# Optimization experiments

Measured on AMD Instinct MI355X. Metric: run time of the kernel, lower is better.

Reference implementation:

```python
import jax, jax.numpy as jnp
import numpy as np

PLANE_SIZE = 512
N_LEVELS = 8
FEATURE_DIM = 16
N_PTS = 524288


def setup_inputs() -> dict:
    key = jax.random.key(0)
    k1, k2, k3 = jax.random.split(key, 3)
    x = jax.random.uniform(k1, (N_PTS, 3), dtype=jnp.float32)
    # per-point float mip level bias in [0, n_levels-1]
    level = jax.random.uniform(k2, (N_PTS, 1), dtype=jnp.float32) * (N_LEVELS - 1)
    fm = jax.random.uniform(k3, (3, PLANE_SIZE, PLANE_SIZE, FEATURE_DIM),
                            minval=-0.01, maxval=0.01, dtype=jnp.float32)
    return {"x": x, "level": level, "fm": fm, "n_levels": N_LEVELS}


def _bilinear(flat_pyr, offsets, sizes, uv, lvl_i):
    # flat_pyr: (3, T, C) concatenated mip levels; uv: (3, N, 2); lvl_i: (3, N) int32
    size = sizes[lvl_i]                      # (3, N) texture size at this mip
    fsize = size.astype(uv.dtype)
    px = uv[..., 0] * fsize - 0.5            # u -> width axis (nvdiffrast convention)
    py = uv[..., 1] * fsize - 0.5            # v -> height axis
    x0 = jnp.floor(px)
    y0 = jnp.floor(py)
    fx = (px - x0)[..., None]
    fy = (py - y0)[..., None]
    x0i = x0.astype(jnp.int32)
    y0i = y0.astype(jnp.int32)
    xa = jnp.clip(x0i, 0, size - 1)          # boundary_mode='clamp'
    xb = jnp.clip(x0i + 1, 0, size - 1)
    ya = jnp.clip(y0i, 0, size - 1)
    yb = jnp.clip(y0i + 1, 0, size - 1)
    base = offsets[lvl_i]
    p = jnp.arange(3)[:, None]
    g = lambda yy, xx: flat_pyr[p, base + yy * size + xx]   # (3, N, C) gather
    f00 = g(ya, xa); f01 = g(ya, xb); f10 = g(yb, xa); f11 = g(yb, xb)
    return (f00 * (1 - fx) + f01 * fx) * (1 - fy) + (f10 * (1 - fx) + f11 * fx) * fy


def reference(x, level, fm, n_levels):
    N = x.shape[0]
    C = fm.shape[-1]
    # build mip pyramid via 2x2 box filter (nvdiffrast auto-mips)
    levels = [fm]
    for _ in range(n_levels - 1):
        t = levels[-1]
        s = t.shape[1]
        levels.append(t.reshape(3, s // 2, 2, s // 2, 2, C).mean(axis=(2, 4)))
    sizes_list = [l.shape[1] for l in levels]
    offsets = jnp.asarray(np.cumsum([0] + [s * s for s in sizes_list[:-1]]), jnp.int32)
    sizes = jnp.asarray(sizes_list, jnp.int32)
    flat_pyr = jnp.concatenate([l.reshape(3, -1, C) for l in levels], axis=1)  # (3, T, C)
    # tri-plane decomposition: plane0 sees (y,z), plane1 (x,z), plane2 (x,y)
    uv = jnp.stack([x[:, [1, 2]], x[:, [0, 2]], x[:, [0, 1]]], axis=0)  # (3, N, 2)
    max_mip = n_levels - 1
    lvl = jnp.clip(jnp.broadcast_to(level.reshape(1, N), (3, N)), 0.0, float(max_mip))
    l0 = jnp.floor(lvl)
    f = (lvl - l0)[..., None]                # (3, N, 1) level fraction
    l0i = l0.astype(jnp.int32)
    l1i = jnp.minimum(l0i + 1, max_mip)
    s0 = _bilinear(flat_pyr, offsets, sizes, uv, l0i)
    s1 = _bilinear(flat_pyr, offsets, sizes, uv, l1i)
    enc = s0 * (1 - f) + s1 * f              # (3, N, C) trilinear (mip-lerped)
    # permute(1,2,0,3).view(N, 3C): per point, concat plane0|plane1|plane2 features
    return jnp.transpose(enc, (1, 0, 2)).reshape(N, 3 * C)
```

## Files before the change

kernel.cpp:

```cpp
#include <hip/hip_runtime.h>
#include <hip/hip_fp16.h>


typedef float  f4v   __attribute__((ext_vector_type(4)));
typedef unsigned int u32x2 __attribute__((ext_vector_type(2)));

#define FM_PLANE_STRIDE (262144 * 16)
#define WS_PLANE_STRIDE (87376 * 16)
#define PSTRIDE_H (349520 * 16)
#define WS_H_BYTES (3ull * PSTRIDE_H * 2ull)

__device__ __forceinline__ unsigned lvl_off(int l) {
    return (1048576u - (1048576u >> (2 * l))) / 3u;
}

__device__ __forceinline__ f4v ld4(const float* p) {
    return *reinterpret_cast<const f4v*>(p);
}
__device__ __forceinline__ f4v ld4nt(const float* p) {
    return __builtin_nontemporal_load(reinterpret_cast<const f4v*>(p));
}
__device__ __forceinline__ void st4(float* p, f4v v) {
    *reinterpret_cast<f4v*>(p) = v;
}
__device__ __forceinline__ void st4nt(float* p, f4v v) {
    __builtin_nontemporal_store(v, reinterpret_cast<f4v*>(p));
}
__device__ __forceinline__ f4v ldraw_h(const __half* p) {
    return *reinterpret_cast<const f4v*>(p);
}
__device__ __forceinline__ u32x2 pack4(f4v v) {
    __half2 lo = __floats2half2_rn(v.x, v.y);
    __half2 hi = __floats2half2_rn(v.z, v.w);
    u32x2 r;
    r.x = *reinterpret_cast<unsigned*>(&lo);
    r.y = *reinterpret_cast<unsigned*>(&hi);
    return r;
}
__device__ __forceinline__ f4v h4f(const __half* p) {
    u32x2 u = *reinterpret_cast<const u32x2*>(p);
    unsigned a0 = u.x, a1 = u.y;
    __half2 lo = *reinterpret_cast<__half2*>(&a0);
    __half2 hi = *reinterpret_cast<__half2*>(&a1);
    float2 flo = __half22float2(lo), fhi = __half22float2(hi);
    f4v r; r.x = flo.x; r.y = flo.y; r.z = fhi.x; r.w = fhi.y;
    return r;
}
__device__ __forceinline__ float2 up2(float rawcomp) {
    unsigned u = __float_as_uint(rawcomp);
    __half2 hh = *reinterpret_cast<__half2*>(&u);
    return __half22float2(hh);
}


__global__ __launch_bounds__(256) void mip_convert_l1(
    const float* __restrict__ fm, __half* __restrict__ wsh)
{
    int t = blockIdx.x * 256 + threadIdx.x;
    const int p = blockIdx.y;
    const int q = t & 3, idx = t >> 2;
    const int y = idx >> 8, x = idx & 255;
    const float* sp = fm + (size_t)p * FM_PLANE_STRIDE
                         + ((size_t)(2 * y) * 512 + 2 * x) * 16 + q * 4;
    f4v a = ld4nt(sp);
    f4v b = ld4nt(sp + 16);
    f4v c = ld4nt(sp + 512 * 16);
    f4v d = ld4nt(sp + 512 * 16 + 16);
    __half* L0 = wsh + (size_t)p * PSTRIDE_H;
    size_t o00 = ((size_t)(2 * y) * 512 + 2 * x) * 16 + q * 4;
    *reinterpret_cast<u32x2*>(L0 + o00)                = pack4(a);
    *reinterpret_cast<u32x2*>(L0 + o00 + 16)           = pack4(b);
    *reinterpret_cast<u32x2*>(L0 + o00 + 512 * 16)     = pack4(c);
    *reinterpret_cast<u32x2*>(L0 + o00 + 512 * 16 + 16) = pack4(d);
    f4v m = (a + b + c + d) * 0.25f;
    __half* L1 = wsh + (size_t)p * PSTRIDE_H + (size_t)262144 * 16;
    *reinterpret_cast<u32x2*>(L1 + ((size_t)y * 256 + x) * 16 + q * 4) = pack4(m);
}

__global__ __launch_bounds__(256) void mip_tail_h(__half* __restrict__ wsh)
{
    const int tile = blockIdx.x;
    const int q    = blockIdx.y;
    const int p    = blockIdx.z;
    const int ty = tile >> 2, tx = tile & 3;
    const int tid = threadIdx.x;

    __shared__ f4v A[32 * 32];
    __shared__ f4v B[16 * 16];

    __half* plane = wsh + (size_t)p * PSTRIDE_H;
    const __half* L1 = plane + (size_t)lvl_off(1) * 16;
    __half* L2 = plane + (size_t)lvl_off(2) * 16;
    __half* L3 = plane + (size_t)lvl_off(3) * 16;
    __half* L4 = plane + (size_t)lvl_off(4) * 16;
    __half* L5 = plane + (size_t)lvl_off(5) * 16;
    __half* L6 = plane + (size_t)lvl_off(6) * 16;
    __half* L7 = plane + (size_t)lvl_off(7) * 16;

    #pragma unroll
    for (int k = 0; k < 4; ++k) {
        int li = tid + k * 256;
        int ly = li >> 5, lx = li & 31;
        int gy = ty * 32 + ly, gx = tx * 32 + lx;
        const __half* sp = L1 + ((size_t)(2 * gy) * 256 + 2 * gx) * 16 + q * 4;
        f4v r = (h4f(sp) + h4f(sp + 16) + h4f(sp + 256 * 16) + h4f(sp + 256 * 16 + 16)) * 0.25f;
        A[li] = r;
        *reinterpret_cast<u32x2*>(L2 + ((size_t)gy * 128 + gx) * 16 + q * 4) = pack4(r);
    }
    __syncthreads();

    {
        int ly = tid >> 4, lx = tid & 15;
        f4v r = (A[(2 * ly) * 32 + 2 * lx]     + A[(2 * ly) * 32 + 2 * lx + 1] +
                 A[(2 * ly + 1) * 32 + 2 * lx] + A[(2 * ly + 1) * 32 + 2 * lx + 1]) * 0.25f;
        B[tid] = r;
        *reinterpret_cast<u32x2*>(L3 + ((size_t)(ty * 16 + ly) * 64 + tx * 16 + lx) * 16 + q * 4) = pack4(r);
    }
    __syncthreads();

    if (tid < 64) {
        int ly = tid >> 3, lx = tid & 7;
        f4v r = (B[(2 * ly) * 16 + 2 * lx]     + B[(2 * ly) * 16 + 2 * lx + 1] +
                 B[(2 * ly + 1) * 16 + 2 * lx] + B[(2 * ly + 1) * 16 + 2 * lx + 1]) * 0.25f;
        A[tid] = r;
        *reinterpret_cast<u32x2*>(L4 + ((size_t)(ty * 8 + ly) * 32 + tx * 8 + lx) * 16 + q * 4) = pack4(r);
    }
    __syncthreads();

    if (tid < 16) {
        int ly = tid >> 2, lx = tid & 3;
        f4v r = (A[(2 * ly) * 8 + 2 * lx]     + A[(2 * ly) * 8 + 2 * lx + 1] +
                 A[(2 * ly + 1) * 8 + 2 * lx] + A[(2 * ly + 1) * 8 + 2 * lx + 1]) * 0.25f;
        B[tid] = r;
        *reinterpret_cast<u32x2*>(L5 + ((size_t)(ty * 4 + ly) * 16 + tx * 4 + lx) * 16 + q * 4) = pack4(r);
    }
    __syncthreads();

    if (tid < 4) {
        int ly = tid >> 1, lx = tid & 1;
        f4v r = (B[(2 * ly) * 4 + 2 * lx]     + B[(2 * ly) * 4 + 2 * lx + 1] +
                 B[(2 * ly + 1) * 4 + 2 * lx] + B[(2 * ly + 1) * 4 + 2 * lx + 1]) * 0.25f;
        A[tid] = r;
        *reinterpret_cast<u32x2*>(L6 + ((size_t)(ty * 2 + ly) * 8 + tx * 2 + lx) * 16 + q * 4) = pack4(r);
    }
    __syncthreads();

    if (tid == 0) {
        f4v r = (A[0] + A[1] + A[2] + A[3]) * 0.25f;
        *reinterpret_cast<u32x2*>(L7 + ((size_t)ty * 4 + tx) * 16 + q * 4) = pack4(r);
    }
}

__device__ __forceinline__ void bilerp8(
    const __half* __restrict__ wsh, int p, int l, float u, float v, int h, float* o)
{
    const int sz = 512 >> l;
    const float fsz = (float)sz;
    float px = u * fsz - 0.5f;
    float py = v * fsz - 0.5f;
    float xf = floorf(px), yf = floorf(py);
    float fx = px - xf, fy = py - yf;
    int xi = (int)xf, yi = (int)yf;
    int xa = min(max(xi, 0), sz - 1);
    int xb = min(xi + 1, sz - 1);
    int ya = min(max(yi, 0), sz - 1);
    int yb = min(yi + 1, sz - 1);
    const __half* base = wsh + (size_t)p * PSTRIDE_H + (size_t)lvl_off(l) * 16 + h * 8;
    const __half* r0 = base + (size_t)(ya * sz) * 16;
    const __half* r1 = base + (size_t)(yb * sz) * 16;
    f4v q00 = ldraw_h(r0 + (size_t)xa * 16);
    f4v q01 = ldraw_h(r0 + (size_t)xb * 16);
    f4v q10 = ldraw_h(r1 + (size_t)xa * 16);
    f4v q11 = ldraw_h(r1 + (size_t)xb * 16);
    float gx = 1.f - fx, gy = 1.f - fy;
    float w00 = gx * gy, w01 = fx * gy, w10 = gx * fy, w11 = fx * fy;
    #pragma unroll
    for (int i = 0; i < 4; ++i) {
        float2 a = up2(q00[i]), b = up2(q01[i]), c = up2(q10[i]), d = up2(q11[i]);
        o[2 * i]     = a.x * w00 + b.x * w01 + c.x * w10 + d.x * w11;
        o[2 * i + 1] = a.y * w00 + b.y * w01 + c.y * w10 + d.y * w11;
    }
}

__global__ __launch_bounds__(256) void trimip_sample_h(
    const float* __restrict__ xyz, const float* __restrict__ level,
    const __half* __restrict__ wsh, float* __restrict__ out, int N)
{
    int t = blockIdx.x * blockDim.x + threadIdx.x;
    if (t >= N * 6) return;
    const int h = t & 1;
    const int r = t >> 1;
    const int n = r / 3;
    const int p = r - n * 3;

    const float c0 = xyz[n * 3 + 0];
    const float c1 = xyz[n * 3 + 1];
    const float c2 = xyz[n * 3 + 2];
    const float u = (p == 0) ? c1 : c0;
    const float v = (p == 2) ? c1 : c2;

    float lv = level[n];
    lv = fminf(fmaxf(lv, 0.f), 7.f);
    float lf = floorf(lv);
    float f = lv - lf;
    int l0 = (int)lf;
    int l1 = min(l0 + 1, 7);

    float s0[8], s1[8];
    bilerp8(wsh, p, l0, u, v, h, s0);
    bilerp8(wsh, p, l1, u, v, h, s1);
    float g = 1.f - f;
    f4v oa, ob;
    #pragma unroll
    for (int i = 0; i < 4; ++i) {
        oa[i] = s0[i] * g + s1[i] * f;
        ob[i] = s0[4 + i] * g + s1[4 + i] * f;
    }
    st4nt(out + (size_t)t * 8, oa);
    st4nt(out + (size_t)t * 8 + 4, ob);
}


__device__ __forceinline__ f4v avg4(f4v a, f4v b, f4v c, f4v d) {
    return (a + b + c + d) * 0.25f;
}

__global__ __launch_bounds__(256) void mip_build_f(
    const float* __restrict__ src, float* __restrict__ dst)
{
    int t = blockIdx.x * blockDim.x + threadIdx.x;
    const int p = blockIdx.y;
    const int q = t & 3, idx = t >> 2;
    const int y = idx >> 8, x = idx & 255;
    const float* sp = src + (size_t)p * FM_PLANE_STRIDE
                          + ((size_t)(2 * y) * 512 + 2 * x) * 16 + q * 4;
    f4v r = avg4(ld4(sp), ld4(sp + 16), ld4(sp + 512 * 16), ld4(sp + 512 * 16 + 16));
    st4(dst + (size_t)p * WS_PLANE_STRIDE + ((size_t)y * 256 + x) * 16 + q * 4, r);
}

__global__ __launch_bounds__(256) void mip_tail_f(float* __restrict__ mips)
{
    const int tile = blockIdx.x, q = blockIdx.y, p = blockIdx.z;
    const int ty = tile >> 2, tx = tile & 3;
    const int tid = threadIdx.x;
    __shared__ f4v A[32 * 32];
    __shared__ f4v B[16 * 16];
    float* plane = mips + (size_t)p * WS_PLANE_STRIDE;
    const float* L1 = plane;
    float* L2 = plane + (size_t)65536 * 16;
    float* L3 = plane + (size_t)81920 * 16;
    float* L4 = plane + (size_t)86016 * 16;
    float* L5 = plane + (size_t)87040 * 16;
    float* L6 = plane + (size_t)87296 * 16;
    float* L7 = plane + (size_t)87360 * 16;

    #pragma unroll
    for (int k = 0; k < 4; ++k) {
        int li = tid + k * 256;
        int ly = li >> 5, lx = li & 31;
        int gy = ty * 32 + ly, gx = tx * 32 + lx;
        const float* sp = L1 + ((size_t)(2 * gy) * 256 + 2 * gx) * 16 + q * 4;
        f4v r = avg4(ld4(sp), ld4(sp + 16), ld4(sp + 256 * 16), ld4(sp + 256 * 16 + 16));
        A[li] = r;
        st4(L2 + ((size_t)gy * 128 + gx) * 16 + q * 4, r);
    }
    __syncthreads();
    {
        int ly = tid >> 4, lx = tid & 15;
        f4v r = avg4(A[(2 * ly) * 32 + 2 * lx],     A[(2 * ly) * 32 + 2 * lx + 1],
                     A[(2 * ly + 1) * 32 + 2 * lx], A[(2 * ly + 1) * 32 + 2 * lx + 1]);
        B[tid] = r;
        st4(L3 + ((size_t)(ty * 16 + ly) * 64 + tx * 16 + lx) * 16 + q * 4, r);
    }
    __syncthreads();
    if (tid < 64) {
        int ly = tid >> 3, lx = tid & 7;
        f4v r = avg4(B[(2 * ly) * 16 + 2 * lx],     B[(2 * ly) * 16 + 2 * lx + 1],
                     B[(2 * ly + 1) * 16 + 2 * lx], B[(2 * ly + 1) * 16 + 2 * lx + 1]);
        A[tid] = r;
        st4(L4 + ((size_t)(ty * 8 + ly) * 32 + tx * 8 + lx) * 16 + q * 4, r);
    }
    __syncthreads();
    if (tid < 16) {
        int ly = tid >> 2, lx = tid & 3;
        f4v r = avg4(A[(2 * ly) * 8 + 2 * lx],     A[(2 * ly) * 8 + 2 * lx + 1],
                     A[(2 * ly + 1) * 8 + 2 * lx], A[(2 * ly + 1) * 8 + 2 * lx + 1]);
        B[tid] = r;
        st4(L5 + ((size_t)(ty * 4 + ly) * 16 + tx * 4 + lx) * 16 + q * 4, r);
    }
    __syncthreads();
    if (tid < 4) {
        int ly = tid >> 1, lx = tid & 1;
        f4v r = avg4(B[(2 * ly) * 4 + 2 * lx],     B[(2 * ly) * 4 + 2 * lx + 1],
                     B[(2 * ly + 1) * 4 + 2 * lx], B[(2 * ly + 1) * 4 + 2 * lx + 1]);
        A[tid] = r;
        st4(L6 + ((size_t)(ty * 2 + ly) * 8 + tx * 2 + lx) * 16 + q * 4, r);
    }
    __syncthreads();
    if (tid == 0) {
        f4v r = avg4(A[0], A[1], A[2], A[3]);
        st4(L7 + ((size_t)ty * 4 + tx) * 16 + q * 4, r);
    }
}

__device__ __forceinline__ f4v bilerp_f(
    const float* __restrict__ fm, const float* __restrict__ mips,
    int p, int l, float u, float v, int q)
{
    const int sz = 512 >> l;
    const float fsz = (float)sz;
    float px = u * fsz - 0.5f;
    float py = v * fsz - 0.5f;
    float xf = floorf(px), yf = floorf(py);
    float fx = px - xf, fy = py - yf;
    int xi = (int)xf, yi = (int)yf;
    int xa = min(max(xi, 0), sz - 1);
    int xb = min(xi + 1, sz - 1);
    int ya = min(max(yi, 0), sz - 1);
    int yb = min(yi + 1, sz - 1);
    const float* base;
    if (l == 0) {
        base = fm + (size_t)p * FM_PLANE_STRIDE;
    } else {
        unsigned off = (262144u - ((unsigned)(sz * sz) << 2)) / 3u;
        base = mips + (size_t)p * WS_PLANE_STRIDE + (size_t)off * 16;
    }
    const float* r0 = base + (size_t)(ya * sz) * 16 + q * 4;
    const float* r1 = base + (size_t)(yb * sz) * 16 + q * 4;
    f4v f00 = ld4(r0 + xa * 16);
    f4v f01 = ld4(r0 + xb * 16);
    f4v f10 = ld4(r1 + xa * 16);
    f4v f11 = ld4(r1 + xb * 16);
    float gx = 1.f - fx, gy = 1.f - fy;
    return (f00 * gx + f01 * fx) * gy + (f10 * gx + f11 * fx) * fy;
}

__global__ __launch_bounds__(256) void trimip_sample_f(
    const float* __restrict__ xyz, const float* __restrict__ level,
    const float* __restrict__ fm, const float* __restrict__ mips,
    float* __restrict__ out, int N)
{
    int t = blockIdx.x * blockDim.x + threadIdx.x;
    if (t >= N * 12) return;
    const int q = t & 3;
    const int r = t >> 2;
    const int n = r / 3;
    const int p = r - n * 3;
    const float c0 = xyz[n * 3 + 0];
    const float c1 = xyz[n * 3 + 1];
    const float c2 = xyz[n * 3 + 2];
    const float u = (p == 0) ? c1 : c0;
    const float v = (p == 2) ? c1 : c2;
    float lv = level[n];
    lv = fminf(fmaxf(lv, 0.f), 7.f);
    float lf = floorf(lv);
    float f = lv - lf;
    int l0 = (int)lf;
    int l1 = min(l0 + 1, 7);
    f4v s0 = bilerp_f(fm, mips, p, l0, u, v, q);
    f4v s1 = bilerp_f(fm, mips, p, l1, u, v, q);
    f4v o = s0 * (1.f - f) + s1 * f;
    st4nt(out + (size_t)t * 4, o);
}

extern "C" void kernel_launch(void* const* d_in, const int* in_sizes, int n_in,
                              void* d_out, int out_size, void* d_ws, size_t ws_size,
                              hipStream_t stream) {
    const float* xyz   = (const float*)d_in[0];
    const float* level = (const float*)d_in[1];
    const float* fm    = (const float*)d_in[2];
    float* out = (float*)d_out;
    const int N = in_sizes[1];

    if (ws_size >= WS_H_BYTES) {
        __half* wsh = (__half*)d_ws;
        mip_convert_l1<<<dim3(1024, 3), dim3(256), 0, stream>>>(fm, wsh);
        mip_tail_h<<<dim3(16, 4, 3), dim3(256), 0, stream>>>(wsh);
        const int total = N * 6;
        trimip_sample_h<<<(total + 255) / 256, 256, 0, stream>>>(xyz, level, wsh, out, N);
    } else {
        float* mips = (float*)d_ws;
        mip_build_f<<<dim3(1024, 3), dim3(256), 0, stream>>>(fm, mips);
        mip_tail_f<<<dim3(16, 4, 3), dim3(256), 0, stream>>>(mips);
        const int total = N * 12;
        trimip_sample_f<<<(total + 255) / 256, 256, 0, stream>>>(xyz, level, fm, mips, out, N);
    }
}
```

Measured before the change: 203.6 us.

## Stage coarsest mip levels in shared memory for the sampling kernel

Each block of the sampling kernel now copies mip levels 5–7 of all three planes (about 32 KB of fp16) into shared memory, and bilinear taps at those levels read from LDS instead of global memory. Block size grows from 256 to 512 threads to spread the staging cost over more points. The aim is to cut global and L2 traffic for the small, heavily reused coarse levels. The cost is a fixed 32 KB load plus a barrier per block, lower occupancy from the shared-memory footprint, and a divergent branch inside each bilinear lookup.

Result: no change. 201.2 us (-1.1%).

```diff
diff --git a/kernel.cpp b/kernel.cpp
--- a/kernel.cpp
+++ b/kernel.cpp
@@ -2,13 +2,15 @@
 #include <hip/hip_fp16.h>
 
 
-typedef float  f4v   __attribute__((ext_vector_type(4)));
+typedef float        f4v   __attribute__((ext_vector_type(4)));
 typedef unsigned int u32x2 __attribute__((ext_vector_type(2)));
+typedef unsigned int u32x4 __attribute__((ext_vector_type(4)));
 
 #define FM_PLANE_STRIDE (262144 * 16)
 #define WS_PLANE_STRIDE (87376 * 16)
 #define PSTRIDE_H (349520 * 16)
 #define WS_H_BYTES (3ull * PSTRIDE_H * 2ull)
+#define LVL5_OFF 349184u
 
 __device__ __forceinline__ unsigned lvl_off(int l) {
     return (1048576u - (1048576u >> (2 * l))) / 3u;
@@ -68,9 +70,9 @@
     f4v d = ld4nt(sp + 512 * 16 + 16);
     __half* L0 = wsh + (size_t)p * PSTRIDE_H;
     size_t o00 = ((size_t)(2 * y) * 512 + 2 * x) * 16 + q * 4;
-    *reinterpret_cast<u32x2*>(L0 + o00)                = pack4(a);
-    *reinterpret_cast<u32x2*>(L0 + o00 + 16)           = pack4(b);
-    *reinterpret_cast<u32x2*>(L0 + o00 + 512 * 16)     = pack4(c);
+    *reinterpret_cast<u32x2*>(L0 + o00)                 = pack4(a);
+    *reinterpret_cast<u32x2*>(L0 + o00 + 16)            = pack4(b);
+    *reinterpret_cast<u32x2*>(L0 + o00 + 512 * 16)      = pack4(c);
     *reinterpret_cast<u32x2*>(L0 + o00 + 512 * 16 + 16) = pack4(d);
     f4v m = (a + b + c + d) * 0.25f;
     __half* L1 = wsh + (size_t)p * PSTRIDE_H + (size_t)262144 * 16;
@@ -152,7 +154,8 @@
 }
 
 __device__ __forceinline__ void bilerp8(
-    const __half* __restrict__ wsh, int p, int l, float u, float v, int h, float* o)
+    const __half* __restrict__ wsh, const __half* __restrict__ lds_h,
+    int p, int l, float u, float v, int h, float* o)
 {
     const int sz = 512 >> l;
     const float fsz = (float)sz;
@@ -165,13 +168,25 @@
     int xb = min(xi + 1, sz - 1);
     int ya = min(max(yi, 0), sz - 1);
     int yb = min(yi + 1, sz - 1);
-    const __half* base = wsh + (size_t)p * PSTRIDE_H + (size_t)lvl_off(l) * 16 + h * 8;
-    const __half* r0 = base + (size_t)(ya * sz) * 16;
-    const __half* r1 = base + (size_t)(yb * sz) * 16;
-    f4v q00 = ldraw_h(r0 + (size_t)xa * 16);
-    f4v q01 = ldraw_h(r0 + (size_t)xb * 16);
-    f4v q10 = ldraw_h(r1 + (size_t)xa * 16);
-    f4v q11 = ldraw_h(r1 + (size_t)xb * 16);
+    f4v q00, q01, q10, q11;
+    if (l >= 5) {
+        const int sel = (l == 6) ? 256 : ((l == 7) ? 320 : 0);
+        const __half* base = lds_h + (size_t)(p * 336 + sel) * 16 + h * 8;
+        const __half* r0 = base + (ya * sz) * 16;
+        const __half* r1 = base + (yb * sz) * 16;
+        q00 = ldraw_h(r0 + xa * 16);
+        q01 = ldraw_h(r0 + xb * 16);
+        q10 = ldraw_h(r1 + xa * 16);
+        q11 = ldraw_h(r1 + xb * 16);
+    } else {
+        const __half* base = wsh + (size_t)p * PSTRIDE_H + (size_t)lvl_off(l) * 16 + h * 8;
+        const __half* r0 = base + (size_t)(ya * sz) * 16;
+        const __half* r1 = base + (size_t)(yb * sz) * 16;
+        q00 = ldraw_h(r0 + (size_t)xa * 16);
+        q01 = ldraw_h(r0 + (size_t)xb * 16);
+        q10 = ldraw_h(r1 + (size_t)xa * 16);
+        q11 = ldraw_h(r1 + (size_t)xb * 16);
+    }
     float gx = 1.f - fx, gy = 1.f - fy;
     float w00 = gx * gy, w01 = fx * gy, w10 = gx * fy, w11 = fx * fy;
     #pragma unroll
@@ -182,11 +197,21 @@
     }
 }
 
-__global__ __launch_bounds__(256) void trimip_sample_h(
+__global__ __launch_bounds__(512) void trimip_sample_h(
     const float* __restrict__ xyz, const float* __restrict__ level,
     const __half* __restrict__ wsh, float* __restrict__ out, int N)
 {
-    int t = blockIdx.x * blockDim.x + threadIdx.x;
+    __shared__ u32x4 lds[2016];
+    for (int uidx = threadIdx.x; uidx < 2016; uidx += 512) {
+        int p = uidx / 672;
+        int rem = uidx - p * 672;
+        lds[uidx] = *reinterpret_cast<const u32x4*>(
+            wsh + (size_t)p * PSTRIDE_H + (size_t)LVL5_OFF * 16 + (size_t)rem * 8);
+    }
+    __syncthreads();
+    const __half* lds_h = reinterpret_cast<const __half*>(lds);
+
+    int t = blockIdx.x * 512 + threadIdx.x;
     if (t >= N * 6) return;
     const int h = t & 1;
     const int r = t >> 1;
@@ -207,8 +232,8 @@
     int l1 = min(l0 + 1, 7);
 
     float s0[8], s1[8];
-    bilerp8(wsh, p, l0, u, v, h, s0);
-    bilerp8(wsh, p, l1, u, v, h, s1);
+    bilerp8(wsh, lds_h, p, l0, u, v, h, s0);
+    bilerp8(wsh, lds_h, p, l1, u, v, h, s1);
     float g = 1.f - f;
     f4v oa, ob;
     #pragma unroll
@@ -377,7 +402,7 @@
         mip_convert_l1<<<dim3(1024, 3), dim3(256), 0, stream>>>(fm, wsh);
         mip_tail_h<<<dim3(16, 4, 3), dim3(256), 0, stream>>>(wsh);
         const int total = N * 6;
-        trimip_sample_h<<<(total + 255) / 256, 256, 0, stream>>>(xyz, level, wsh, out, N);
+        trimip_sample_h<<<(total + 511) / 512, 512, 0, stream>>>(xyz, level, wsh, out, N);
     } else {
         float* mips = (float*)d_ws;
         mip_build_f<<<dim3(1024, 3), dim3(256), 0, stream>>>(fm, mips);
```

## Sort points by Morton key and level before sampling; read level 0 from fp32 input

Applied to the files above, without the earlier changes.

Adds a counting sort that bins points by a 16^3 Morton cell and integer mip level (histogram, single-block scan, atomic scatter), then samples in sorted order with a per-plane grid so neighbouring threads hit nearby texels. The fp16 copy of level 0 is no longer written; level 0 is bilinearly sampled directly from the fp32 input, which shrinks the pyramid build traffic. The sort is meant to improve cache locality of the random gathers. In exchange it adds four extra launches, atomics, and scattered output writes through the sort index.

After: 288.7 us. +41.8%, slower.

```diff
diff --git a/kernel.cpp b/kernel.cpp
--- a/kernel.cpp
+++ b/kernel.cpp
@@ -2,16 +2,18 @@
 #include <hip/hip_fp16.h>
 
 
-typedef float  f4v   __attribute__((ext_vector_type(4)));
+typedef float        f4v   __attribute__((ext_vector_type(4)));
 typedef unsigned int u32x2 __attribute__((ext_vector_type(2)));
 
 #define FM_PLANE_STRIDE (262144 * 16)
+#define PW_STRIDE_H (87376 * 16)
+#define PYR_BYTES 8388608ull
 #define WS_PLANE_STRIDE (87376 * 16)
-#define PSTRIDE_H (349520 * 16)
-#define WS_H_BYTES (3ull * PSTRIDE_H * 2ull)
-
-__device__ __forceinline__ unsigned lvl_off(int l) {
-    return (1048576u - (1048576u >> (2 * l))) / 3u;
+#define NBINS 32768
+
+__device__ __forceinline__ unsigned lvl_off_ws(int l) {
+    const int sz = 512 >> l;
+    return (262144u - ((unsigned)(sz * sz) << 2)) / 3u;
 }
 
 __device__ __forceinline__ f4v ld4(const float* p) {
@@ -51,10 +53,26 @@
     __half2 hh = *reinterpret_cast<__half2*>(&u);
     return __half22float2(hh);
 }
-
-
-__global__ __launch_bounds__(256) void mip_convert_l1(
-    const float* __restrict__ fm, __half* __restrict__ wsh)
+__device__ __forceinline__ unsigned part1by2(unsigned v) {
+    v = (v | (v << 16)) & 0x030000FFu;
+    v = (v | (v << 8))  & 0x0300F00Fu;
+    v = (v | (v << 4))  & 0x030C30C3u;
+    v = (v | (v << 2))  & 0x09249249u;
+    return v;
+}
+__device__ __forceinline__ unsigned point_key(float x, float y, float z, float lv) {
+    int xi = min(max((int)(x * 16.f), 0), 15);
+    int yi = min(max((int)(y * 16.f), 0), 15);
+    int zi = min(max((int)(z * 16.f), 0), 15);
+    int l0 = (int)lv;
+    unsigned m = part1by2((unsigned)xi) | (part1by2((unsigned)yi) << 1)
+               | (part1by2((unsigned)zi) << 2);
+    return ((unsigned)l0 << 12) | m;
+}
+
+
+__global__ __launch_bounds__(256) void mip_l1_h(
+    const float* __restrict__ fm, __half* __restrict__ pyr)
 {
     int t = blockIdx.x * 256 + threadIdx.x;
     const int p = blockIdx.y;
@@ -66,18 +84,12 @@
     f4v b = ld4nt(sp + 16);
     f4v c = ld4nt(sp + 512 * 16);
     f4v d = ld4nt(sp + 512 * 16 + 16);
-    __half* L0 = wsh + (size_t)p * PSTRIDE_H;
-    size_t o00 = ((size_t)(2 * y) * 512 + 2 * x) * 16 + q * 4;
-    *reinterpret_cast<u32x2*>(L0 + o00)                = pack4(a);
-    *reinterpret_cast<u32x2*>(L0 + o00 + 16)           = pack4(b);
-    *reinterpret_cast<u32x2*>(L0 + o00 + 512 * 16)     = pack4(c);
-    *reinterpret_cast<u32x2*>(L0 + o00 + 512 * 16 + 16) = pack4(d);
     f4v m = (a + b + c + d) * 0.25f;
-    __half* L1 = wsh + (size_t)p * PSTRIDE_H + (size_t)262144 * 16;
+    __half* L1 = pyr + (size_t)p * PW_STRIDE_H;
     *reinterpret_cast<u32x2*>(L1 + ((size_t)y * 256 + x) * 16 + q * 4) = pack4(m);
 }
 
-__global__ __launch_bounds__(256) void mip_tail_h(__half* __restrict__ wsh)
+__global__ __launch_bounds__(256) void mip_tail_h(__half* __restrict__ pyr)
 {
     const int tile = blockIdx.x;
     const int q    = blockIdx.y;
@@ -88,14 +100,14 @@
     __shared__ f4v A[32 * 32];
     __shared__ f4v B[16 * 16];
 
-    __half* plane = wsh + (size_t)p * PSTRIDE_H;
-    const __half* L1 = plane + (size_t)lvl_off(1) * 16;
-    __half* L2 = plane + (size_t)lvl_off(2) * 16;
-    __half* L3 = plane + (size_t)lvl_off(3) * 16;
-    __half* L4 = plane + (size_t)lvl_off(4) * 16;
-    __half* L5 = plane + (size_t)lvl_off(5) * 16;
-    __half* L6 = plane + (size_t)lvl_off(6) * 16;
-    __half* L7 = plane + (size_t)lvl_off(7) * 16;
+    __half* plane = pyr + (size_t)p * PW_STRIDE_H;
+    const __half* L1 = plane;
+    __half* L2 = plane + (size_t)65536 * 16;
+    __half* L3 = plane + (size_t)81920 * 16;
+    __half* L4 = plane + (size_t)86016 * 16;
+    __half* L5 = plane + (size_t)87040 * 16;
+    __half* L6 = plane + (size_t)87296 * 16;
+    __half* L7 = plane + (size_t)87360 * 16;
 
     #pragma unroll
     for (int k = 0; k < 4; ++k) {
@@ -151,8 +163,90 @@
     }
 }
 
-__device__ __forceinline__ void bilerp8(
-    const __half* __restrict__ wsh, int p, int l, float u, float v, int h, float* o)
+
+__global__ __launch_bounds__(256) void hist_build(
+    const float* __restrict__ xyz, const float* __restrict__ level,
+    unsigned* __restrict__ hist, int N)
+{
+    int n = blockIdx.x * 256 + threadIdx.x;
+    if (n >= N) return;
+    float x = xyz[n * 3], y = xyz[n * 3 + 1], z = xyz[n * 3 + 2];
+    float lv = fminf(fmaxf(level[n], 0.f), 7.f);
+    atomicAdd(&hist[point_key(x, y, z, lv)], 1u);
+}
+
+__global__ __launch_bounds__(1024) void scan_hist(unsigned* __restrict__ hist)
+{
+    __shared__ unsigned s[1024];
+    const unsigned tid = threadIdx.x;
+    const unsigned base = tid * 32;
+    unsigned sum = 0;
+    #pragma unroll
+    for (int k = 0; k < 32; ++k) sum += hist[base + k];
+    s[tid] = sum;
+    __syncthreads();
+    for (unsigned off = 1; off < 1024; off <<= 1) {
+        unsigned v = (tid >= off) ? s[tid - off] : 0u;
+        __syncthreads();
+        s[tid] += v;
+        __syncthreads();
+    }
+    unsigned run = s[tid] - sum;
+    #pragma unroll
+    for (int k = 0; k < 32; ++k) {
+        unsigned h = hist[base + k];
+        hist[base + k] = run;
+        run += h;
+    }
+}
+
+__global__ __launch_bounds__(256) void scatter_pts(
+    const float* __restrict__ xyz, const float* __restrict__ level,
+    unsigned* __restrict__ hist, float* __restrict__ spos,
+    unsigned* __restrict__ sidx, int N)
+{
+    int n = blockIdx.x * 256 + threadIdx.x;
+    if (n >= N) return;
+    float x = xyz[n * 3], y = xyz[n * 3 + 1], z = xyz[n * 3 + 2];
+    float lv = fminf(fmaxf(level[n], 0.f), 7.f);
+    unsigned pos = atomicAdd(&hist[point_key(x, y, z, lv)], 1u);
+    f4v v; v.x = x; v.y = y; v.z = z; v.w = lv;
+    st4nt(spos + (size_t)pos * 4, v);
+    __builtin_nontemporal_store(n, (int*)&sidx[pos]);
+}
+
+
+__device__ __forceinline__ void bilerp_l0(
+    const float* __restrict__ fm, int p, float u, float v, int h, float* o)
+{
+    float px = u * 512.f - 0.5f;
+    float py = v * 512.f - 0.5f;
+    float xf = floorf(px), yf = floorf(py);
+    float fx = px - xf, fy = py - yf;
+    int xi = (int)xf, yi = (int)yf;
+    int xa = min(max(xi, 0), 511);
+    int xb = min(xi + 1, 511);
+    int ya = min(max(yi, 0), 511);
+    int yb = min(yi + 1, 511);
+    const float* base = fm + (size_t)p * FM_PLANE_STRIDE + h * 8;
+    const float* p00 = base + ((size_t)ya * 512 + xa) * 16;
+    const float* p01 = base + ((size_t)ya * 512 + xb) * 16;
+    const float* p10 = base + ((size_t)yb * 512 + xa) * 16;
+    const float* p11 = base + ((size_t)yb * 512 + xb) * 16;
+    f4v a0 = ld4(p00), a1 = ld4(p00 + 4);
+    f4v b0 = ld4(p01), b1 = ld4(p01 + 4);
+    f4v c0 = ld4(p10), c1 = ld4(p10 + 4);
+    f4v d0 = ld4(p11), d1 = ld4(p11 + 4);
+    float gx = 1.f - fx, gy = 1.f - fy;
+    float w00 = gx * gy, w01 = fx * gy, w10 = gx * fy, w11 = fx * fy;
+    f4v lo = a0 * w00 + b0 * w01 + c0 * w10 + d0 * w11;
+    f4v hi = a1 * w00 + b1 * w01 + c1 * w10 + d1 * w11;
+    #pragma unroll
+    for (int i = 0; i < 4; ++i) { o[i] = lo[i]; o[4 + i] = hi[i]; }
+}
+
+__device__ __forceinline__ void bilerp_h(
+    const __half* __restrict__ pyr, int p, int l, float u, float v, int h, float* o)
 {
     const int sz = 512 >> l;
     const float fsz = (float)sz;
@@ -165,7 +259,7 @@
     int xb = min(xi + 1, sz - 1);
     int ya = min(max(yi, 0), sz - 1);
     int yb = min(yi + 1, sz - 1);
-    const __half* base = wsh + (size_t)p * PSTRIDE_H + (size_t)lvl_off(l) * 16 + h * 8;
+    const __half* base = pyr + (size_t)p * PW_STRIDE_H + (size_t)lvl_off_ws(l) * 16 + h * 8;
     const __half* r0 = base + (size_t)(ya * sz) * 16;
     const __half* r1 = base + (size_t)(yb * sz) * 16;
     f4v q00 = ldraw_h(r0 + (size_t)xa * 16);
@@ -182,33 +276,33 @@
     }
 }
 
-__global__ __launch_bounds__(256) void trimip_sample_h(
-    const float* __restrict__ xyz, const float* __restrict__ level,
-    const __half* __restrict__ wsh, float* __restrict__ out, int N)
-{
-    int t = blockIdx.x * blockDim.x + threadIdx.x;
-    if (t >= N * 6) return;
-    const int h = t & 1;
-    const int r = t >> 1;
-    const int n = r / 3;
-    const int p = r - n * 3;
-
-    const float c0 = xyz[n * 3 + 0];
-    const float c1 = xyz[n * 3 + 1];
-    const float c2 = xyz[n * 3 + 2];
-    const float u = (p == 0) ? c1 : c0;
-    const float v = (p == 2) ? c1 : c2;
-
-    float lv = level[n];
-    lv = fminf(fmaxf(lv, 0.f), 7.f);
+__global__ __launch_bounds__(256) void trimip_sample_sorted(
+    const float* __restrict__ spos, const unsigned* __restrict__ sidx,
+    const float* __restrict__ fm, const __half* __restrict__ pyr,
+    float* __restrict__ out, int N)
+{
+    int tl = blockIdx.x * 256 + threadIdx.x;
+    if (tl >= 2 * N) return;
+    const int h = tl & 1;
+    const int rank = tl >> 1;
+    const int p = blockIdx.y;
+
+    f4v sp = ld4(spos + (size_t)rank * 4);
+    const unsigned n = sidx[rank];
+    const float u = (p == 0) ? sp.y : sp.x;
+    const float v = (p == 2) ? sp.y : sp.z;
+    const float lv = sp.w;
+
     float lf = floorf(lv);
     float f = lv - lf;
     int l0 = (int)lf;
     int l1 = min(l0 + 1, 7);
 
     float s0[8], s1[8];
-    bilerp8(wsh, p, l0, u, v, h, s0);
-    bilerp8(wsh, p, l1, u, v, h, s1);
+    if (l0 == 0) bilerp_l0(fm, p, u, v, h, s0);
+    else         bilerp_h(pyr, p, l0, u, v, h, s0);
+    bilerp_h(pyr, p, l1, u, v, h, s1);
+
     float g = 1.f - f;
     f4v oa, ob;
     #pragma unroll
@@ -216,12 +310,13 @@
         oa[i] = s0[i] * g + s1[i] * f;
         ob[i] = s0[4 + i] * g + s1[4 + i] * f;
     }
-    st4nt(out + (size_t)t * 8, oa);
-    st4nt(out + (size_t)t * 8 + 4, ob);
-}
-
-
-__device__ __forceinline__ f4v avg4(f4v a, f4v b, f4v c, f4v d) {
+    float* op = out + (size_t)n * 48 + p * 16 + h * 8;
+    st4nt(op, oa);
+    st4nt(op + 4, ob);
+}
+
+
+__device__ __forceinline__ f4v avg4f(f4v a, f4v b, f4v c, f4v d) {
     return (a + b + c + d) * 0.25f;
 }
 
@@ -234,7 +329,7 @@
     const int y = idx >> 8, x = idx & 255;
     const float* sp = src + (size_t)p * FM_PLANE_STRIDE
                           + ((size_t)(2 * y) * 512 + 2 * x) * 16 + q * 4;
-    f4v r = avg4(ld4(sp), ld4(sp + 16), ld4(sp + 512 * 16), ld4(sp + 512 * 16 + 16));
+    f4v r = avg4f(ld4(sp), ld4(sp + 16), ld4(sp + 512 * 16), ld4(sp + 512 * 16 + 16));
     st4(dst + (size_t)p * WS_PLANE_STRIDE + ((size_t)y * 256 + x) * 16 + q * 4, r);
 }
 
@@ -260,45 +355,45 @@
         int ly = li >> 5, lx = li & 31;
         int gy = ty * 32 + ly, gx = tx * 32 + lx;
         const float* sp = L1 + ((size_t)(2 * gy) * 256 + 2 * gx) * 16 + q * 4;
-        f4v r = avg4(ld4(sp), ld4(sp + 16), ld4(sp + 256 * 16), ld4(sp + 256 * 16 + 16));
+        f4v r = avg4f(ld4(sp), ld4(sp + 16), ld4(sp + 256 * 16), ld4(sp + 256 * 16 + 16));
         A[li] = r;
         st4(L2 + ((size_t)gy * 128 + gx) * 16 + q * 4, r);
     }
     __syncthreads();
     {
         int ly = tid >> 4, lx = tid & 15;
-        f4v r = avg4(A[(2 * ly) * 32 + 2 * lx],     A[(2 * ly) * 32 + 2 * lx + 1],
-                     A[(2 * ly + 1) * 32 + 2 * lx], A[(2 * ly + 1) * 32 + 2 * lx + 1]);
+        f4v r = avg4f(A[(2 * ly) * 32 + 2 * lx],     A[(2 * ly) * 32 + 2 * lx + 1],
+                      A[(2 * ly + 1) * 32 + 2 * lx], A[(2 * ly + 1) * 32 + 2 * lx + 1]);
         B[tid] = r;
         st4(L3 + ((size_t)(ty * 16 + ly) * 64 + tx * 16 + lx) * 16 + q * 4, r);
     }
     __syncthreads();
     if (tid < 64) {
         int ly = tid >> 3, lx = tid & 7;
-        f4v r = avg4(B[(2 * ly) * 16 + 2 * lx],     B[(2 * ly) * 16 + 2 * lx + 1],
-                     B[(2 * ly + 1) * 16 + 2 * lx], B[(2 * ly + 1) * 16 + 2 * lx + 1]);
+        f4v r = avg4f(B[(2 * ly) * 16 + 2 * lx],     B[(2 * ly) * 16 + 2 * lx + 1],
+                      B[(2 * ly + 1) * 16 + 2 * lx], B[(2 * ly + 1) * 16 + 2 * lx + 1]);
         A[tid] = r;
         st4(L4 + ((size_t)(ty * 8 + ly) * 32 + tx * 8 + lx) * 16 + q * 4, r);
     }
     __syncthreads();
     if (tid < 16) {
         int ly = tid >> 2, lx = tid & 3;
-        f4v r = avg4(A[(2 * ly) * 8 + 2 * lx],     A[(2 * ly) * 8 + 2 * lx + 1],
-                     A[(2 * ly + 1) * 8 + 2 * lx], A[(2 * ly + 1) * 8 + 2 * lx + 1]);
+        f4v r = avg4f(A[(2 * ly) * 8 + 2 * lx],     A[(2 * ly) * 8 + 2 * lx + 1],
+                      A[(2 * ly + 1) * 8 + 2 * lx], A[(2 * ly + 1) * 8 + 2 * lx + 1]);
         B[tid] = r;
         st4(L5 + ((size_t)(ty * 4 + ly) * 16 + tx * 4 + lx) * 16 + q * 4, r);
     }
     __syncthreads();
     if (tid < 4) {
         int ly = tid >> 1, lx = tid & 1;
-        f4v r = avg4(B[(2 * ly) * 4 + 2 * lx],     B[(2 * ly) * 4 + 2 * lx + 1],
-                     B[(2 * ly + 1) * 4 + 2 * lx], B[(2 * ly + 1) * 4 + 2 * lx + 1]);
+        f4v r = avg4f(B[(2 * ly) * 4 + 2 * lx],     B[(2 * ly) * 4 + 2 * lx + 1],
+                      B[(2 * ly + 1) * 4 + 2 * lx], B[(2 * ly + 1) * 4 + 2 * lx + 1]);
         A[tid] = r;
         st4(L6 + ((size_t)(ty * 2 + ly) * 8 + tx * 2 + lx) * 16 + q * 4, r);
     }
     __syncthreads();
     if (tid == 0) {
-        f4v r = avg4(A[0], A[1], A[2], A[3]);
+        f4v r = avg4f(A[0], A[1], A[2], A[3]);
         st4(L7 + ((size_t)ty * 4 + tx) * 16 + q * 4, r);
     }
 }
@@ -351,8 +446,7 @@
     const float c2 = xyz[n * 3 + 2];
     const float u = (p == 0) ? c1 : c0;
     const float v = (p == 2) ? c1 : c2;
-    float lv = level[n];
-    lv = fminf(fmaxf(lv, 0.f), 7.f);
+    float lv = fminf(fmaxf(level[n], 0.f), 7.f);
     float lf = floorf(lv);
     float f = lv - lf;
     int l0 = (int)lf;
@@ -372,17 +466,32 @@
     float* out = (float*)d_out;
     const int N = in_sizes[1];
 
-    if (ws_size >= WS_H_BYTES) {
-        __half* wsh = (__half*)d_ws;
-        mip_convert_l1<<<dim3(1024, 3), dim3(256), 0, stream>>>(fm, wsh);
-        mip_tail_h<<<dim3(16, 4, 3), dim3(256), 0, stream>>>(wsh);
-        const int total = N * 6;
-        trimip_sample_h<<<(total + 255) / 256, 256, 0, stream>>>(xyz, level, wsh, out, N);
+    const size_t sposOff = PYR_BYTES;
+    const size_t sidxOff = sposOff + (size_t)N * 16;
+    const size_t histOff = sidxOff + (size_t)N * 4;
+    const size_t needed  = histOff + NBINS * 4;
+
+    if (ws_size >= needed) {
+        char* ws = (char*)d_ws;
+        __half*   pyr  = (__half*)ws;
+        float*    spos = (float*)(ws + sposOff);
+        unsigned* sidx = (unsigned*)(ws + sidxOff);
+        unsigned* hist = (unsigned*)(ws + histOff);
+        const int nb = (N + 255) / 256;
+
+        hipMemsetAsync(hist, 0, NBINS * 4, stream);
+        mip_l1_h<<<dim3(1024, 3), dim3(256), 0, stream>>>(fm, pyr);
+        mip_tail_h<<<dim3(16, 4, 3), dim3(256), 0, stream>>>(pyr);
+        hist_build<<<nb, 256, 0, stream>>>(xyz, level, hist, N);
+        scan_hist<<<1, 1024, 0, stream>>>(hist);
+        scatter_pts<<<nb, 256, 0, stream>>>(xyz, level, hist, spos, sidx, N);
+        trimip_sample_sorted<<<dim3((2 * N + 255) / 256, 3), dim3(256), 0, stream>>>(
+            spos, sidx, fm, pyr, out, N);
     } else {
         float* mips = (float*)d_ws;
         mip_build_f<<<dim3(1024, 3), dim3(256), 0, stream>>>(fm, mips);
         mip_tail_f<<<dim3(16, 4, 3), dim3(256), 0, stream>>>(mips);
-        const int total = N * 12;
-        trimip_sample_f<<<(total + 255) / 256, 256, 0, stream>>>(xyz, level, fm, mips, out, N);
-    }
-}
+        trimip_sample_f<<<(N * 12 + 255) / 256, 256, 0, stream>>>(
+            xyz, level, fm, mips, out, N);
+    }
+}
```
